# Kernel tuning notes

Measured on AMD Instinct MI355X. Metric: run time of the kernel, lower is better.

The kernel has to match this reference:

```python
import jax, jax.numpy as jnp
import numpy as np

B, N1, N2, D = 4096, 16, 32, 30   # node batch, 1st-hop nbrs, 2nd-hop nbrs, nodeDataLen
H, HD = 6, 5                       # heads, head_dim (embed_dim = size_out*heads = 30)
LH = 64                            # linear_hidden
NEG_SLOPE = 0.02


def setup_inputs() -> dict:
    key = jax.random.key(0)
    ks = jax.random.split(key, 20)
    def w(k, shape, std=0.2):
        return jax.random.normal(k, shape, dtype=jnp.float32) * std
    return {
        "x2": jax.random.normal(ks[0], (B, N1, N2, D), dtype=jnp.float32),
        "self_feat": jax.random.normal(ks[1], (B, D), dtype=jnp.float32),
        # second-hop GraphLayer params (size_in=30 -> embed 30)
        "lin_w2": w(ks[2], (D, D)), "lin_b2": jnp.zeros((D,), jnp.float32),
        "in_w2": w(ks[3], (3 * D, D), 0.1), "in_b2": jnp.zeros((3 * D,), jnp.float32),
        "out_w2": w(ks[4], (D, D), 0.1), "out_b2": jnp.zeros((D,), jnp.float32),
        # first-hop GraphLayer params
        "lin_w1": w(ks[5], (D, D)), "lin_b1": jnp.zeros((D,), jnp.float32),
        "in_w1": w(ks[6], (3 * D, D), 0.1), "in_b1": jnp.zeros((3 * D,), jnp.float32),
        "out_w1": w(ks[7], (D, D), 0.1), "out_b1": jnp.zeros((D,), jnp.float32),
        # classification MLP
        "cw1": w(ks[8], (LH, D), 0.02), "cb1": jnp.zeros((LH,), jnp.float32),
        "cw2": w(ks[9], (LH, LH), 0.02), "cb2": jnp.zeros((LH,), jnp.float32),
        "cw3": w(ks[10], (2, LH), 0.02), "cb3": jnp.zeros((2,), jnp.float32),
    }


def graph_layer(x, lw, lb, iw, ib, ow, ob):
    """x: [S, D] -> Linear + LeakyReLU(0.02) + MHA(self) + mean over S -> [D].
    Dropout(0.2) is identity in eval mode."""
    S = x.shape[0]
    y = jax.nn.leaky_relu(x @ lw.T + lb, NEG_SLOPE)          # [S, D]
    qkv = y @ iw.T + ib                                       # [S, 3D] packed in_proj
    q, k, v = jnp.split(qkv, 3, axis=-1)
    q = q.reshape(S, H, HD)
    k = k.reshape(S, H, HD)
    v = v.reshape(S, H, HD)
    scores = jnp.einsum('shd,thd->hst', q, k) / np.float32(np.sqrt(HD))
    att = jax.nn.softmax(scores, axis=-1)                     # [H, S, S]
    o = jnp.einsum('hst,thd->shd', att, v).reshape(S, H * HD) # [S, D]
    o = o @ ow.T + ob
    return o.mean(axis=0)                                     # [D]


def reference(x2, self_feat,
              lin_w2, lin_b2, in_w2, in_b2, out_w2, out_b2,
              lin_w1, lin_b1, in_w1, in_b1, out_w1, out_b1,
              cw1, cb1, cw2, cb2, cw3, cb3):
    gl2 = lambda x: graph_layer(x, lin_w2, lin_b2, in_w2, in_b2, out_w2, out_b2)
    h1 = jax.vmap(jax.vmap(gl2))(x2)                          # [B, N1, D] second-hop aggregation
    seq = jnp.concatenate([h1, self_feat[:, None, :]], axis=1)  # [B, N1+1, D] append current node
    gl1 = lambda x: graph_layer(x, lin_w1, lin_b1, in_w1, in_b1, out_w1, out_b1)
    emb = jax.vmap(gl1)(seq)                                  # [B, D]
    h = jax.nn.leaky_relu(emb @ cw1.T + cb1, NEG_SLOPE)
    h = jax.nn.leaky_relu(h @ cw2.T + cb2, NEG_SLOPE)
    logits = h @ cw3.T + cb3                                  # [B, 2]
    # original applies Softmax(dim=0) to the 1-D 2-vector per node == softmax over classes
    return jax.nn.softmax(logits, axis=-1)
```

## Files before the change

### kernel.cpp

```cpp
#include <hip/hip_runtime.h>
#include <math.h>

#define LRELU(v) fmaxf((v), 0.02f * (v))

typedef __attribute__((ext_vector_type(8)))  short short8;
typedef __attribute__((ext_vector_type(4)))  float f32x4;
typedef __attribute__((ext_vector_type(16))) float f32x16;
typedef __attribute__((ext_vector_type(2)))  int   int2v;
typedef __attribute__((ext_vector_type(4)))  int   int4v;

__device__ inline short f2bf(float f) {
    unsigned u = __builtin_bit_cast(unsigned, f);
    unsigned r = (u + 0x7FFFu + ((u >> 16) & 1u)) >> 16;
    return (short)r;
}
__device__ inline int cvt_pk_bf16(float lo, float hi) {
    int r;
    asm("v_cvt_pk_bf16_f32 %0, %1, %2" : "=v"(r) : "v"(lo), "v"(hi));
    return r;
}
__device__ inline float exp2_asm(float x) {
    float r;
    asm("v_exp_f32 %0, %1" : "=v"(r) : "v"(x));
    return r;
}

#define PAIRS 8
#define RS5L  0.6451994329f

__global__ __launch_bounds__(256, 5) void gl2_kernel(
    const float* __restrict__ x2,
    const float* __restrict__ lw, const float* __restrict__ lb,
    const float* __restrict__ iw, const float* __restrict__ ib,
    const float* __restrict__ ow, const float* __restrict__ ob,
    float* __restrict__ h1out)
{
    __shared__ __attribute__((aligned(16))) short y_lds[32][40];
    __shared__ __attribute__((aligned(16))) short qmf[6][33][8];
    __shared__ __attribute__((aligned(16))) short kmf[6][33][8];
    __shared__ __attribute__((aligned(16))) short vbf[6][8][40];
    __shared__ float obar[32];

    const int tid  = threadIdx.x;
    const int lane = tid & 63;
    const int w    = tid >> 6;
    const int l15  = lane & 15;
    const int lq   = lane >> 4;
    const int h5   = lane >> 5;
    const int scol = lane & 31;
    const int rowz = (lane < 32) ? scol : 32;

    for (int i = tid; i < 792; i += 256) { ((int*)qmf)[i] = 0; ((int*)kmf)[i] = 0; }
    for (int i = tid; i < 960; i += 256) ((int*)vbf)[i] = 0;
    if (tid < 2) obar[30 + tid] = 0.0f;

    const int di = w & 1, si = w >> 1;
    short8 blw; float lbv;
    {
        int d = di * 16 + l15;
        #pragma unroll
        for (int i = 0; i < 8; ++i) {
            int k = lq * 8 + i;
            blw[i] = f2bf((d < 30 && k < 30) ? lw[d * 30 + k] : 0.0f);
        }
        lbv = (d < 30) ? lb[d] : 0.0f;
    }
    const int jtA = (3 * w) >> 1, jtB = (3 * w + 2) >> 1;
    short8 biwA, biwB; float ibvA, ibvB;
    {
        int jA = jtA * 16 + l15, jB = jtB * 16 + l15;
        #pragma unroll
        for (int i = 0; i < 8; ++i) {
            int k = lq * 8 + i;
            biwA[i] = f2bf((jA < 90 && k < 30) ? iw[jA * 30 + k] : 0.0f);
            biwB[i] = f2bf((jB < 90 && k < 30) ? iw[jB * 30 + k] : 0.0f);
        }
        ibvA = (jA < 90) ? ib[jA] : 0.0f;
        ibvB = (jB < 90) ? ib[jB] : 0.0f;
    }
    __syncthreads();

    for (int p = 0; p < PAIRS; ++p) {
        const long pair = (long)blockIdx.x * PAIRS + p;
        const float* xp = x2 + pair * 960;

        {
            int s = si * 16 + l15;
            const float* xr = xp + s * 30 + lq * 8;
            float xv[8];
            #pragma unroll
            for (int i = 0; i < 8; ++i) {
                int k = lq * 8 + i;
                xv[i] = (k < 30) ? xr[i] : 0.0f;
            }
            int4v ai;
            ai.x = cvt_pk_bf16(xv[0], xv[1]);
            ai.y = cvt_pk_bf16(xv[2], xv[3]);
            ai.z = cvt_pk_bf16(xv[4], xv[5]);
            ai.w = cvt_pk_bf16(xv[6], xv[7]);
            short8 af = __builtin_bit_cast(short8, ai);
            f32x4 c = {0.0f, 0.0f, 0.0f, 0.0f};
            c = __builtin_amdgcn_mfma_f32_16x16x32_bf16(af, blw, c, 0, 0, 0);
            float y0 = LRELU(c[0] + lbv), y1 = LRELU(c[1] + lbv);
            float y2 = LRELU(c[2] + lbv), y3 = LRELU(c[3] + lbv);
            int p01 = cvt_pk_bf16(y0, y1), p23 = cvt_pk_bf16(y2, y3);
            int row = si * 16 + lq * 4, col = di * 16 + l15;
            y_lds[row + 0][col] = (short)p01;
            y_lds[row + 1][col] = (short)(p01 >> 16);
            y_lds[row + 2][col] = (short)p23;
            y_lds[row + 3][col] = (short)(p23 >> 16);
        }
        __syncthreads();

        {
            short8 a0 = *(const short8*)&y_lds[l15][lq * 8];
            short8 a1 = *(const short8*)&y_lds[16 + l15][lq * 8];
            #pragma unroll
            for (int t = 0; t < 3; ++t) {
                int T = 3 * w + t, jt = T >> 1, si_ = T & 1;
                short8 a = si_ ? a1 : a0;
                short8 b = (jt == jtA) ? biwA : biwB;
                float ibv = (jt == jtA) ? ibvA : ibvB;
                f32x4 c = {0.0f, 0.0f, 0.0f, 0.0f};
                c = __builtin_amdgcn_mfma_f32_16x16x32_bf16(a, b, c, 0, 0, 0);
                int j = jt * 16 + l15;
                int s0 = si_ * 16 + lq * 4;
                if (j < 30) {
                    int h = j / 5, e = j - 5 * h;
                    int p01 = cvt_pk_bf16(c[0] + ibv, c[1] + ibv);
                    int p23 = cvt_pk_bf16(c[2] + ibv, c[3] + ibv);
                    qmf[h][s0 + 0][e] = (short)p01;
                    qmf[h][s0 + 1][e] = (short)(p01 >> 16);
                    qmf[h][s0 + 2][e] = (short)p23;
                    qmf[h][s0 + 3][e] = (short)(p23 >> 16);
                } else if (j < 60) {
                    int jj = j - 30; int h = jj / 5, e = jj - 5 * h;
                    float ibl = ibv * RS5L;
                    int p01 = cvt_pk_bf16(fmaf(c[0], RS5L, ibl), fmaf(c[1], RS5L, ibl));
                    int p23 = cvt_pk_bf16(fmaf(c[2], RS5L, ibl), fmaf(c[3], RS5L, ibl));
                    kmf[h][s0 + 0][e] = (short)p01;
                    kmf[h][s0 + 1][e] = (short)(p01 >> 16);
                    kmf[h][s0 + 2][e] = (short)p23;
                    kmf[h][s0 + 3][e] = (short)(p23 >> 16);
                } else if (j < 90) {
                    int jj = j - 60; int h = jj / 5, e = jj - 5 * h;
                    int k0 = ((s0 >> 1) & 4) | ((s0 << 1) & 8) | (s0 & 16);
                    int2v wv;
                    wv.x = cvt_pk_bf16(c[0] + ibv, c[1] + ibv);
                    wv.y = cvt_pk_bf16(c[2] + ibv, c[3] + ibv);
                    *(int2v*)&vbf[h][e][k0] = wv;
                }
            }
        }
        __syncthreads();

        if (w < 3) {
            #pragma unroll
            for (int hh = 0; hh < 2; ++hh) {
                const int h = 2 * w + hh;
                short8 af = *(const short8*)&kmf[h][rowz][0];
                short8 bf = *(const short8*)&qmf[h][rowz][0];
                f32x16 c;
                #pragma unroll
                for (int r = 0; r < 16; ++r) c[r] = 0.0f;
                c = __builtin_amdgcn_mfma_f32_32x32x16_bf16(af, bf, c, 0, 0, 0);
                float m = c[0];
                #pragma unroll
                for (int r = 1; r < 16; ++r) m = fmaxf(m, c[r]);
                m = fmaxf(m, __shfl_xor(m, 32));
                float Z = 0.0f;
                #pragma unroll
                for (int r = 0; r < 16; ++r) { c[r] = exp2_asm(c[r] - m); Z += c[r]; }
                Z += __shfl_xor(Z, 32);
                float rZ = __builtin_amdgcn_rcpf(Z) * (1.0f / 32.0f);
                int4v a1i, a2i;
                a1i.x = cvt_pk_bf16(c[0] * rZ,  c[1] * rZ);
                a1i.y = cvt_pk_bf16(c[2] * rZ,  c[3] * rZ);
                a1i.z = cvt_pk_bf16(c[4] * rZ,  c[5] * rZ);
                a1i.w = cvt_pk_bf16(c[6] * rZ,  c[7] * rZ);
                a2i.x = cvt_pk_bf16(c[8] * rZ,  c[9] * rZ);
                a2i.y = cvt_pk_bf16(c[10] * rZ, c[11] * rZ);
                a2i.z = cvt_pk_bf16(c[12] * rZ, c[13] * rZ);
                a2i.w = cvt_pk_bf16(c[14] * rZ, c[15] * rZ);
                short8 b1 = *(const short8*)&vbf[h][scol & 7][8 * h5];
                short8 b2 = *(const short8*)&vbf[h][scol & 7][16 + 8 * h5];
                f32x16 P;
                #pragma unroll
                for (int r = 0; r < 16; ++r) P[r] = 0.0f;
                P = __builtin_amdgcn_mfma_f32_32x32x16_bf16(
                        __builtin_bit_cast(short8, a1i), b1, P, 0, 0, 0);
                P = __builtin_amdgcn_mfma_f32_32x32x16_bf16(
                        __builtin_bit_cast(short8, a2i), b2, P, 0, 0, 0);
                float sm = 0.0f;
                #pragma unroll
                for (int r = 0; r < 16; ++r) sm += P[r];
                sm += __shfl_xor(sm, 32);
                if (lane < 5) obar[h * 5 + lane] = sm;
            }
        }
        __syncthreads();

        if (tid < 240) {
            const int d = tid >> 3, jq = tid & 7;
            f32x4 ov = *(const f32x4*)&obar[jq * 4];
            float part = 0.0f;
            #pragma unroll
            for (int i = 0; i < 4; ++i) {
                int j = jq * 4 + i;
                if (j < 30) part = fmaf(ov[i], ow[d * 30 + j], part);
            }
            part += __shfl_down(part, 4, 8);
            part += __shfl_down(part, 2, 8);
            part += __shfl_down(part, 1, 8);
            if (jq == 0) h1out[pair * 30 + d] = part + ob[d];
        }
    }
}

__global__ __launch_bounds__(256, 5) void gl1_mlp_kernel(
    const float* __restrict__ h1, const float* __restrict__ self_feat,
    const float* __restrict__ lw, const float* __restrict__ lb,
    const float* __restrict__ iw, const float* __restrict__ ib,
    const float* __restrict__ ow, const float* __restrict__ ob,
    const float* __restrict__ cw1, const float* __restrict__ cb1,
    const float* __restrict__ cw2, const float* __restrict__ cb2,
    const float* __restrict__ cw3, const float* __restrict__ cb3,
    float* __restrict__ out)
{
    __shared__ __attribute__((aligned(16))) short y_lds[32][40];
    __shared__ __attribute__((aligned(16))) short qmf[6][33][8];
    __shared__ __attribute__((aligned(16))) short kmf[6][33][8];
    __shared__ __attribute__((aligned(16))) short vbf[6][8][40];
    __shared__ float obar[32];
    __shared__ float embb[32];
    __shared__ float hb1[64];
    __shared__ float hb2[64];
    __shared__ float lg[2];

    const int tid  = threadIdx.x;
    const int lane = tid & 63;
    const int w    = tid >> 6;
    const int l15  = lane & 15;
    const int lq   = lane >> 4;
    const int h5   = lane >> 5;
    const int scol = lane & 31;
    const int rowz = (lane < 32) ? scol : 32;

    for (int i = tid; i < 792; i += 256) { ((int*)qmf)[i] = 0; ((int*)kmf)[i] = 0; }
    for (int i = tid; i < 960; i += 256) ((int*)vbf)[i] = 0;
    if (tid < 2) obar[30 + tid] = 0.0f;

    const int di = w & 1, si = w >> 1;
    short8 blw; float lbv;
    {
        int d = di * 16 + l15;
        #pragma unroll
        for (int i = 0; i < 8; ++i) {
            int k = lq * 8 + i;
            blw[i] = f2bf((d < 30 && k < 30) ? lw[d * 30 + k] : 0.0f);
        }
        lbv = (d < 30) ? lb[d] : 0.0f;
    }
    const int jtA = (3 * w) >> 1, jtB = (3 * w + 2) >> 1;
    short8 biwA, biwB; float ibvA, ibvB;
    {
        int jA = jtA * 16 + l15, jB = jtB * 16 + l15;
        #pragma unroll
        for (int i = 0; i < 8; ++i) {
            int k = lq * 8 + i;
            biwA[i] = f2bf((jA < 90 && k < 30) ? iw[jA * 30 + k] : 0.0f);
            biwB[i] = f2bf((jB < 90 && k < 30) ? iw[jB * 30 + k] : 0.0f);
        }
        ibvA = (jA < 90) ? ib[jA] : 0.0f;
        ibvB = (jB < 90) ? ib[jB] : 0.0f;
    }
    __syncthreads();

    const long node = (long)blockIdx.x;
    const float* h1p = h1 + node * 480;
    const float* sfp = self_feat + node * 30;

    {
        float xv[8];
        if (si == 0) {
            const float* xr = h1p + l15 * 30 + lq * 8;
            #pragma unroll
            for (int i = 0; i < 8; ++i) {
                int k = lq * 8 + i;
                xv[i] = (k < 30) ? xr[i] : 0.0f;
            }
        } else {
            #pragma unroll
            for (int i = 0; i < 8; ++i) {
                int k = lq * 8 + i;
                xv[i] = (l15 == 0 && k < 30) ? sfp[k] : 0.0f;
            }
        }
        int4v ai;
        ai.x = cvt_pk_bf16(xv[0], xv[1]);
        ai.y = cvt_pk_bf16(xv[2], xv[3]);
        ai.z = cvt_pk_bf16(xv[4], xv[5]);
        ai.w = cvt_pk_bf16(xv[6], xv[7]);
        short8 af = __builtin_bit_cast(short8, ai);
        f32x4 c = {0.0f, 0.0f, 0.0f, 0.0f};
        c = __builtin_amdgcn_mfma_f32_16x16x32_bf16(af, blw, c, 0, 0, 0);
        float y0 = LRELU(c[0] + lbv), y1 = LRELU(c[1] + lbv);
        float y2 = LRELU(c[2] + lbv), y3 = LRELU(c[3] + lbv);
        int p01 = cvt_pk_bf16(y0, y1), p23 = cvt_pk_bf16(y2, y3);
        int row = si * 16 + lq * 4, col = di * 16 + l15;
        y_lds[row + 0][col] = (short)p01;
        y_lds[row + 1][col] = (short)(p01 >> 16);
        y_lds[row + 2][col] = (short)p23;
        y_lds[row + 3][col] = (short)(p23 >> 16);
    }
    __syncthreads();

    {
        short8 a0 = *(const short8*)&y_lds[l15][lq * 8];
        short8 a1 = *(const short8*)&y_lds[16 + l15][lq * 8];
        #pragma unroll
        for (int t = 0; t < 3; ++t) {
            int T = 3 * w + t, jt = T >> 1, si_ = T & 1;
            short8 a = si_ ? a1 : a0;
            short8 b = (jt == jtA) ? biwA : biwB;
            float ibv = (jt == jtA) ? ibvA : ibvB;
            f32x4 c = {0.0f, 0.0f, 0.0f, 0.0f};
            c = __builtin_amdgcn_mfma_f32_16x16x32_bf16(a, b, c, 0, 0, 0);
            int j = jt * 16 + l15;
            int s0 = si_ * 16 + lq * 4;
            if (j < 30) {
                int h = j / 5, e = j - 5 * h;
                int p01 = cvt_pk_bf16(c[0] + ibv, c[1] + ibv);
                int p23 = cvt_pk_bf16(c[2] + ibv, c[3] + ibv);
                qmf[h][s0 + 0][e] = (short)p01;
                qmf[h][s0 + 1][e] = (short)(p01 >> 16);
                qmf[h][s0 + 2][e] = (short)p23;
                qmf[h][s0 + 3][e] = (short)(p23 >> 16);
            } else if (j < 60) {
                int jj = j - 30; int h = jj / 5, e = jj - 5 * h;
                float ibl = ibv * RS5L;
                int p01 = cvt_pk_bf16(fmaf(c[0], RS5L, ibl), fmaf(c[1], RS5L, ibl));
                int p23 = cvt_pk_bf16(fmaf(c[2], RS5L, ibl), fmaf(c[3], RS5L, ibl));
                kmf[h][s0 + 0][e] = (short)p01;
                kmf[h][s0 + 1][e] = (short)(p01 >> 16);
                kmf[h][s0 + 2][e] = (short)p23;
                kmf[h][s0 + 3][e] = (short)(p23 >> 16);
            } else if (j < 90) {
                int jj = j - 60; int h = jj / 5, e = jj - 5 * h;
                int k0 = ((s0 >> 1) & 4) | ((s0 << 1) & 8) | (s0 & 16);
                int2v wv;
                wv.x = cvt_pk_bf16(c[0] + ibv, c[1] + ibv);
                wv.y = cvt_pk_bf16(c[2] + ibv, c[3] + ibv);
                *(int2v*)&vbf[h][e][k0] = wv;
            }
        }
    }
    __syncthreads();

    if (w < 3) {
        #pragma unroll
        for (int hh = 0; hh < 2; ++hh) {
            const int h = 2 * w + hh;
            short8 af = *(const short8*)&kmf[h][rowz][0];
            short8 bf = *(const short8*)&qmf[h][rowz][0];
            f32x16 c;
            #pragma unroll
            for (int r = 0; r < 16; ++r) c[r] = 0.0f;
            c = __builtin_amdgcn_mfma_f32_32x32x16_bf16(af, bf, c, 0, 0, 0);
            #pragma unroll
            for (int r = 0; r < 16; ++r) {
                int tr = (r & 3) + 8 * (r >> 2) + 4 * h5;
                c[r] = (tr < 17) ? c[r] : -1e30f;
            }
            float m = c[0];
            #pragma unroll
            for (int r = 1; r < 16; ++r) m = fmaxf(m, c[r]);
            m = fmaxf(m, __shfl_xor(m, 32));
            float Z = 0.0f;
            #pragma unroll
            for (int r = 0; r < 16; ++r) { c[r] = exp2_asm(c[r] - m); Z += c[r]; }
            Z += __shfl_xor(Z, 32);
            float rZ = __builtin_amdgcn_rcpf(Z) * (1.0f / 17.0f);
            int4v a1i, a2i;
            a1i.x = cvt_pk_bf16(c[0] * rZ,  c[1] * rZ);
            a1i.y = cvt_pk_bf16(c[2] * rZ,  c[3] * rZ);
            a1i.z = cvt_pk_bf16(c[4] * rZ,  c[5] * rZ);
            a1i.w = cvt_pk_bf16(c[6] * rZ,  c[7] * rZ);
            a2i.x = cvt_pk_bf16(c[8] * rZ,  c[9] * rZ);
            a2i.y = cvt_pk_bf16(c[10] * rZ, c[11] * rZ);
            a2i.z = cvt_pk_bf16(c[12] * rZ, c[13] * rZ);
            a2i.w = cvt_pk_bf16(c[14] * rZ, c[15] * rZ);
            short8 b1 = *(const short8*)&vbf[h][scol & 7][8 * h5];
            short8 b2 = *(const short8*)&vbf[h][scol & 7][16 + 8 * h5];
            f32x16 P;
            #pragma unroll
            for (int r = 0; r < 16; ++r) P[r] = 0.0f;
            P = __builtin_amdgcn_mfma_f32_32x32x16_bf16(
                    __builtin_bit_cast(short8, a1i), b1, P, 0, 0, 0);
            P = __builtin_amdgcn_mfma_f32_32x32x16_bf16(
                    __builtin_bit_cast(short8, a2i), b2, P, 0, 0, 0);
            float sm = 0.0f;
            #pragma unroll
            for (int r = 0; r < 8; ++r) sm += P[r];
            sm += (h5 == 0) ? P[8] : 0.0f;
            sm += __shfl_xor(sm, 32);
            if (lane < 5) obar[h * 5 + lane] = sm;
        }
    }
    __syncthreads();

    if (tid < 240) {
        const int d = tid >> 3, jq = tid & 7;
        f32x4 ov = *(const f32x4*)&obar[jq * 4];
        float part = 0.0f;
        #pragma unroll
        for (int i = 0; i < 4; ++i) {
            int j = jq * 4 + i;
            if (j < 30) part = fmaf(ov[i], ow[d * 30 + j], part);
        }
        part += __shfl_down(part, 4, 8);
        part += __shfl_down(part, 2, 8);
        part += __shfl_down(part, 1, 8);
        if (jq == 0) embb[d] = part + ob[d];
    }
    __syncthreads();

    {
        const int o = tid >> 2, kq = tid & 3;
        float part = 0.0f;
        #pragma unroll
        for (int i = 0; i < 8; ++i) {
            int k = kq * 8 + i;
            if (k < 30) part = fmaf(embb[k], cw1[o * 30 + k], part);
        }
        part += __shfl_down(part, 2, 4);
        part += __shfl_down(part, 1, 4);
        if (kq == 0) hb1[o] = LRELU(part + cb1[o]);
    }
    __syncthreads();
    {
        const int o = tid >> 2, kq = tid & 3;
        float part = 0.0f;
        #pragma unroll
        for (int i = 0; i < 16; ++i) {
            int k = kq * 16 + i;
            part = fmaf(hb1[k], cw2[o * 64 + k], part);
        }
        part += __shfl_down(part, 2, 4);
        part += __shfl_down(part, 1, 4);
        if (kq == 0) hb2[o] = LRELU(part + cb2[o]);
    }
    __syncthreads();
    if (tid < 128) {
        const int c = tid >> 6, k = tid & 63;
        float part = hb2[k] * cw3[c * 64 + k];
        part += __shfl_down(part, 32);
        part += __shfl_down(part, 16);
        part += __shfl_down(part, 8);
        part += __shfl_down(part, 4);
        part += __shfl_down(part, 2);
        part += __shfl_down(part, 1);
        if (k == 0) lg[c] = part + cb3[c];
    }
    __syncthreads();
    if (tid < 2) {
        float m = fmaxf(lg[0], lg[1]);
        float e0 = __expf(lg[0] - m), e1 = __expf(lg[1] - m);
        float pr = ((tid == 0) ? e0 : e1) / (e0 + e1);
        out[node * 2 + tid] = pr;
    }
}

extern "C" void kernel_launch(void* const* d_in, const int* in_sizes, int n_in,
                              void* d_out, int out_size, void* d_ws, size_t ws_size,
                              hipStream_t stream)
{
    const float* x2        = (const float*)d_in[0];
    const float* self_feat = (const float*)d_in[1];
    const float* lin_w2 = (const float*)d_in[2];
    const float* lin_b2 = (const float*)d_in[3];
    const float* in_w2  = (const float*)d_in[4];
    const float* in_b2  = (const float*)d_in[5];
    const float* out_w2 = (const float*)d_in[6];
    const float* out_b2 = (const float*)d_in[7];
    const float* lin_w1 = (const float*)d_in[8];
    const float* lin_b1 = (const float*)d_in[9];
    const float* in_w1  = (const float*)d_in[10];
    const float* in_b1  = (const float*)d_in[11];
    const float* out_w1 = (const float*)d_in[12];
    const float* out_b1 = (const float*)d_in[13];
    const float* cw1 = (const float*)d_in[14];
    const float* cb1 = (const float*)d_in[15];
    const float* cw2 = (const float*)d_in[16];
    const float* cb2 = (const float*)d_in[17];
    const float* cw3 = (const float*)d_in[18];
    const float* cb3 = (const float*)d_in[19];
    float* outp = (float*)d_out;

    float* h1 = (float*)d_ws;

    gl2_kernel<<<(4096 * 16) / PAIRS, 256, 0, stream>>>(
        x2, lin_w2, lin_b2, in_w2, in_b2, out_w2, out_b2, h1);

    gl1_mlp_kernel<<<4096, 256, 0, stream>>>(
        h1, self_feat, lin_w1, lin_b1, in_w1, in_b1, out_w1, out_b1,
        cw1, cb1, cw2, cb2, cw3, cb3, outp);
}
```

Baseline: 547.1 us.

## Fuse second-hop, first-hop and MLP kernels into one per-node kernel

Merges the two launches into one kernel where each block handles a whole node: it processes its 16 neighbour sets two at a time, with double-width LDS buffers so all four waves share the attention stage (three heads each instead of two heads on three waves). The h1 results stay in shared memory rather than going through a global workspace, and the first-hop layer and MLP then run in the same block. This removes one kernel launch and the h1 write/read round trip, and raises wave utilisation in the attention stage. In exchange it doubles LDS use and adds register pressure from holding both layers' weights, which may lower occupancy.

Result: slower. 585.3 us (+7.0%).

```diff
diff --git a/kernel.cpp b/kernel.cpp
--- a/kernel.cpp
+++ b/kernel.cpp
@@ -25,21 +25,31 @@
     return r;
 }
 
-#define PAIRS 8
 #define RS5L  0.6451994329f
 
-__global__ __launch_bounds__(256, 5) void gl2_kernel(
-    const float* __restrict__ x2,
-    const float* __restrict__ lw, const float* __restrict__ lb,
-    const float* __restrict__ iw, const float* __restrict__ ib,
-    const float* __restrict__ ow, const float* __restrict__ ob,
-    float* __restrict__ h1out)
+__global__ __launch_bounds__(256, 5) void fused_kernel(
+    const float* __restrict__ x2, const float* __restrict__ self_feat,
+    const float* __restrict__ lw2, const float* __restrict__ lb2,
+    const float* __restrict__ iw2, const float* __restrict__ ib2,
+    const float* __restrict__ ow2, const float* __restrict__ ob2,
+    const float* __restrict__ lw1, const float* __restrict__ lb1,
+    const float* __restrict__ iw1, const float* __restrict__ ib1,
+    const float* __restrict__ ow1, const float* __restrict__ ob1,
+    const float* __restrict__ cw1, const float* __restrict__ cb1,
+    const float* __restrict__ cw2, const float* __restrict__ cb2,
+    const float* __restrict__ cw3, const float* __restrict__ cb3,
+    float* __restrict__ out)
 {
-    __shared__ __attribute__((aligned(16))) short y_lds[32][40];
-    __shared__ __attribute__((aligned(16))) short qmf[6][33][8];
-    __shared__ __attribute__((aligned(16))) short kmf[6][33][8];
-    __shared__ __attribute__((aligned(16))) short vbf[6][8][40];
-    __shared__ float obar[32];
+    __shared__ __attribute__((aligned(16))) short y_lds[2][32][40];
+    __shared__ __attribute__((aligned(16))) short qmf[2][6][33][8];
+    __shared__ __attribute__((aligned(16))) short kmf[2][6][33][8];
+    __shared__ __attribute__((aligned(16))) short vbf[2][6][8][40];
+    __shared__ __attribute__((aligned(16))) float h1f[16][33];
+    __shared__ float obar[2][32];
+    __shared__ float embb[32];
+    __shared__ float hb1[64];
+    __shared__ float hb2[64];
+    __shared__ float lg[2];
 
     const int tid  = threadIdx.x;
     const int lane = tid & 63;
@@ -50,116 +60,134 @@
     const int scol = lane & 31;
     const int rowz = (lane < 32) ? scol : 32;
 
-    for (int i = tid; i < 792; i += 256) { ((int*)qmf)[i] = 0; ((int*)kmf)[i] = 0; }
-    for (int i = tid; i < 960; i += 256) ((int*)vbf)[i] = 0;
-    if (tid < 2) obar[30 + tid] = 0.0f;
+    for (int i = tid; i < 1584; i += 256) { ((int*)qmf)[i] = 0; ((int*)kmf)[i] = 0; }
+    for (int i = tid; i < 1920; i += 256) ((int*)vbf)[i] = 0;
+    if (tid < 4) obar[tid >> 1][30 + (tid & 1)] = 0.0f;
 
     const int di = w & 1, si = w >> 1;
-    short8 blw; float lbv;
+    short8 blw2f, blw1f; float lbv2v, lbv1v;
     {
         int d = di * 16 + l15;
         #pragma unroll
         for (int i = 0; i < 8; ++i) {
             int k = lq * 8 + i;
-            blw[i] = f2bf((d < 30 && k < 30) ? lw[d * 30 + k] : 0.0f);
-        }
-        lbv = (d < 30) ? lb[d] : 0.0f;
+            bool ok = (d < 30 && k < 30);
+            blw2f[i] = f2bf(ok ? lw2[d * 30 + k] : 0.0f);
+            blw1f[i] = f2bf(ok ? lw1[d * 30 + k] : 0.0f);
+        }
+        lbv2v = (d < 30) ? lb2[d] : 0.0f;
+        lbv1v = (d < 30) ? lb1[d] : 0.0f;
     }
     const int jtA = (3 * w) >> 1, jtB = (3 * w + 2) >> 1;
-    short8 biwA, biwB; float ibvA, ibvB;
+    short8 biwA2, biwB2, biwA1, biwB1;
+    float ibvA2, ibvB2, ibvA1, ibvB1;
     {
         int jA = jtA * 16 + l15, jB = jtB * 16 + l15;
         #pragma unroll
         for (int i = 0; i < 8; ++i) {
             int k = lq * 8 + i;
-            biwA[i] = f2bf((jA < 90 && k < 30) ? iw[jA * 30 + k] : 0.0f);
-            biwB[i] = f2bf((jB < 90 && k < 30) ? iw[jB * 30 + k] : 0.0f);
-        }
-        ibvA = (jA < 90) ? ib[jA] : 0.0f;
-        ibvB = (jB < 90) ? ib[jB] : 0.0f;
-    }
-    __syncthreads();
-
-    for (int p = 0; p < PAIRS; ++p) {
-        const long pair = (long)blockIdx.x * PAIRS + p;
-        const float* xp = x2 + pair * 960;
+            bool okA = (jA < 90 && k < 30), okB = (jB < 90 && k < 30);
+            biwA2[i] = f2bf(okA ? iw2[jA * 30 + k] : 0.0f);
+            biwB2[i] = f2bf(okB ? iw2[jB * 30 + k] : 0.0f);
+            biwA1[i] = f2bf(okA ? iw1[jA * 30 + k] : 0.0f);
+            biwB1[i] = f2bf(okB ? iw1[jB * 30 + k] : 0.0f);
+        }
+        ibvA2 = (jA < 90) ? ib2[jA] : 0.0f;
+        ibvB2 = (jB < 90) ? ib2[jB] : 0.0f;
+        ibvA1 = (jA < 90) ? ib1[jA] : 0.0f;
+        ibvB1 = (jB < 90) ? ib1[jB] : 0.0f;
+    }
+    __syncthreads();
+
+    const long node = (long)blockIdx.x;
+    const float* xbase = x2 + node * (16L * 960);
+    const float* sfp   = self_feat + node * 30;
+
+    for (int it = 0; it < 8; ++it) {
 
         {
             int s = si * 16 + l15;
-            const float* xr = xp + s * 30 + lq * 8;
-            float xv[8];
-            #pragma unroll
-            for (int i = 0; i < 8; ++i) {
-                int k = lq * 8 + i;
-                xv[i] = (k < 30) ? xr[i] : 0.0f;
-            }
-            int4v ai;
-            ai.x = cvt_pk_bf16(xv[0], xv[1]);
-            ai.y = cvt_pk_bf16(xv[2], xv[3]);
-            ai.z = cvt_pk_bf16(xv[4], xv[5]);
-            ai.w = cvt_pk_bf16(xv[6], xv[7]);
-            short8 af = __builtin_bit_cast(short8, ai);
-            f32x4 c = {0.0f, 0.0f, 0.0f, 0.0f};
-            c = __builtin_amdgcn_mfma_f32_16x16x32_bf16(af, blw, c, 0, 0, 0);
-            float y0 = LRELU(c[0] + lbv), y1 = LRELU(c[1] + lbv);
-            float y2 = LRELU(c[2] + lbv), y3 = LRELU(c[3] + lbv);
-            int p01 = cvt_pk_bf16(y0, y1), p23 = cvt_pk_bf16(y2, y3);
-            int row = si * 16 + lq * 4, col = di * 16 + l15;
-            y_lds[row + 0][col] = (short)p01;
-            y_lds[row + 1][col] = (short)(p01 >> 16);
-            y_lds[row + 2][col] = (short)p23;
-            y_lds[row + 3][col] = (short)(p23 >> 16);
+            #pragma unroll
+            for (int pr = 0; pr < 2; ++pr) {
+                const float* xr = xbase + (2 * it + pr) * 960 + s * 30 + lq * 8;
+                float xv[8];
+                #pragma unroll
+                for (int i = 0; i < 8; ++i) {
+                    int k = lq * 8 + i;
+                    xv[i] = (k < 30) ? xr[i] : 0.0f;
+                }
+                int4v ai;
+                ai.x = cvt_pk_bf16(xv[0], xv[1]);
+                ai.y = cvt_pk_bf16(xv[2], xv[3]);
+                ai.z = cvt_pk_bf16(xv[4], xv[5]);
+                ai.w = cvt_pk_bf16(xv[6], xv[7]);
+                short8 af = __builtin_bit_cast(short8, ai);
+                f32x4 c = {0.0f, 0.0f, 0.0f, 0.0f};
+                c = __builtin_amdgcn_mfma_f32_16x16x32_bf16(af, blw2f, c, 0, 0, 0);
+                float y0 = LRELU(c[0] + lbv2v), y1 = LRELU(c[1] + lbv2v);
+                float y2 = LRELU(c[2] + lbv2v), y3 = LRELU(c[3] + lbv2v);
+                int p01 = cvt_pk_bf16(y0, y1), p23 = cvt_pk_bf16(y2, y3);
+                int row = si * 16 + lq * 4, col = di * 16 + l15;
+                y_lds[pr][row + 0][col] = (short)p01;
+                y_lds[pr][row + 1][col] = (short)(p01 >> 16);
+                y_lds[pr][row + 2][col] = (short)p23;
+                y_lds[pr][row + 3][col] = (short)(p23 >> 16);
+            }
         }
         __syncthreads();
 
         {
-            short8 a0 = *(const short8*)&y_lds[l15][lq * 8];
-            short8 a1 = *(const short8*)&y_lds[16 + l15][lq * 8];
-            #pragma unroll
-            for (int t = 0; t < 3; ++t) {
-                int T = 3 * w + t, jt = T >> 1, si_ = T & 1;
-                short8 a = si_ ? a1 : a0;
-                short8 b = (jt == jtA) ? biwA : biwB;
-                float ibv = (jt == jtA) ? ibvA : ibvB;
-                f32x4 c = {0.0f, 0.0f, 0.0f, 0.0f};
-                c = __builtin_amdgcn_mfma_f32_16x16x32_bf16(a, b, c, 0, 0, 0);
-                int j = jt * 16 + l15;
-                int s0 = si_ * 16 + lq * 4;
-                if (j < 30) {
-                    int h = j / 5, e = j - 5 * h;
-                    int p01 = cvt_pk_bf16(c[0] + ibv, c[1] + ibv);
-                    int p23 = cvt_pk_bf16(c[2] + ibv, c[3] + ibv);
-                    qmf[h][s0 + 0][e] = (short)p01;
-                    qmf[h][s0 + 1][e] = (short)(p01 >> 16);
-                    qmf[h][s0 + 2][e] = (short)p23;
-                    qmf[h][s0 + 3][e] = (short)(p23 >> 16);
-                } else if (j < 60) {
-                    int jj = j - 30; int h = jj / 5, e = jj - 5 * h;
-                    float ibl = ibv * RS5L;
-                    int p01 = cvt_pk_bf16(fmaf(c[0], RS5L, ibl), fmaf(c[1], RS5L, ibl));
-                    int p23 = cvt_pk_bf16(fmaf(c[2], RS5L, ibl), fmaf(c[3], RS5L, ibl));
-                    kmf[h][s0 + 0][e] = (short)p01;
-                    kmf[h][s0 + 1][e] = (short)(p01 >> 16);
-                    kmf[h][s0 + 2][e] = (short)p23;
-                    kmf[h][s0 + 3][e] = (short)(p23 >> 16);
-                } else if (j < 90) {
-                    int jj = j - 60; int h = jj / 5, e = jj - 5 * h;
-                    int k0 = ((s0 >> 1) & 4) | ((s0 << 1) & 8) | (s0 & 16);
-                    int2v wv;
-                    wv.x = cvt_pk_bf16(c[0] + ibv, c[1] + ibv);
-                    wv.y = cvt_pk_bf16(c[2] + ibv, c[3] + ibv);
-                    *(int2v*)&vbf[h][e][k0] = wv;
+            #pragma unroll
+            for (int pr = 0; pr < 2; ++pr) {
+                short8 a0 = *(const short8*)&y_lds[pr][l15][lq * 8];
+                short8 a1 = *(const short8*)&y_lds[pr][16 + l15][lq * 8];
+                #pragma unroll
+                for (int t = 0; t < 3; ++t) {
+                    int T = 3 * w + t, jt = T >> 1, si_ = T & 1;
+                    short8 a = si_ ? a1 : a0;
+                    short8 b = (jt == jtA) ? biwA2 : biwB2;
+                    float ibv = (jt == jtA) ? ibvA2 : ibvB2;
+                    f32x4 c = {0.0f, 0.0f, 0.0f, 0.0f};
+                    c = __builtin_amdgcn_mfma_f32_16x16x32_bf16(a, b, c, 0, 0, 0);
+                    int j = jt * 16 + l15;
+                    int s0 = si_ * 16 + lq * 4;
+                    if (j < 30) {
+                        int h = j / 5, e = j - 5 * h;
+                        int p01 = cvt_pk_bf16(c[0] + ibv, c[1] + ibv);
+                        int p23 = cvt_pk_bf16(c[2] + ibv, c[3] + ibv);
+                        qmf[pr][h][s0 + 0][e] = (short)p01;
+                        qmf[pr][h][s0 + 1][e] = (short)(p01 >> 16);
+                        qmf[pr][h][s0 + 2][e] = (short)p23;
+                        qmf[pr][h][s0 + 3][e] = (short)(p23 >> 16);
+                    } else if (j < 60) {
+                        int jj = j - 30; int h = jj / 5, e = jj - 5 * h;
+                        float ibl = ibv * RS5L;
+                        int p01 = cvt_pk_bf16(fmaf(c[0], RS5L, ibl), fmaf(c[1], RS5L, ibl));
+                        int p23 = cvt_pk_bf16(fmaf(c[2], RS5L, ibl), fmaf(c[3], RS5L, ibl));
+                        kmf[pr][h][s0 + 0][e] = (short)p01;
+                        kmf[pr][h][s0 + 1][e] = (short)(p01 >> 16);
+                        kmf[pr][h][s0 + 2][e] = (short)p23;
+                        kmf[pr][h][s0 + 3][e] = (short)(p23 >> 16);
+                    } else if (j < 90) {
+                        int jj = j - 60; int h = jj / 5, e = jj - 5 * h;
+                        int k0 = ((s0 >> 1) & 4) | ((s0 << 1) & 8) | (s0 & 16);
+                        int2v wv;
+                        wv.x = cvt_pk_bf16(c[0] + ibv, c[1] + ibv);
+                        wv.y = cvt_pk_bf16(c[2] + ibv, c[3] + ibv);
+                        *(int2v*)&vbf[pr][h][e][k0] = wv;
+                    }
                 }
             }
         }
         __syncthreads();
 
-        if (w < 3) {
-            #pragma unroll
-            for (int hh = 0; hh < 2; ++hh) {
-                const int h = 2 * w + hh;
-                short8 af = *(const short8*)&kmf[h][rowz][0];
-                short8 bf = *(const short8*)&qmf[h][rowz][0];
+        {
+            const int pr = w >> 1;
+            #pragma unroll
+            for (int hh = 0; hh < 3; ++hh) {
+                const int h = 3 * (w & 1) + hh;
+                short8 af = *(const short8*)&kmf[pr][h][rowz][0];
+                short8 bf = *(const short8*)&qmf[pr][h][rowz][0];
                 f32x16 c;
                 #pragma unroll
                 for (int r = 0; r < 16; ++r) c[r] = 0.0f;
@@ -182,8 +210,8 @@
                 a2i.y = cvt_pk_bf16(c[10] * rZ, c[11] * rZ);
                 a2i.z = cvt_pk_bf16(c[12] * rZ, c[13] * rZ);
                 a2i.w = cvt_pk_bf16(c[14] * rZ, c[15] * rZ);
-                short8 b1 = *(const short8*)&vbf[h][scol & 7][8 * h5];
-                short8 b2 = *(const short8*)&vbf[h][scol & 7][16 + 8 * h5];
+                short8 b1 = *(const short8*)&vbf[pr][h][scol & 7][8 * h5];
+                short8 b2 = *(const short8*)&vbf[pr][h][scol & 7][16 + 8 * h5];
                 f32x16 P;
                 #pragma unroll
                 for (int r = 0; r < 16; ++r) P[r] = 0.0f;
@@ -195,99 +223,39 @@
                 #pragma unroll
                 for (int r = 0; r < 16; ++r) sm += P[r];
                 sm += __shfl_xor(sm, 32);
-                if (lane < 5) obar[h * 5 + lane] = sm;
+                if (lane < 5) obar[pr][h * 5 + lane] = sm;
             }
         }
         __syncthreads();
 
         if (tid < 240) {
             const int d = tid >> 3, jq = tid & 7;
-            f32x4 ov = *(const f32x4*)&obar[jq * 4];
-            float part = 0.0f;
-            #pragma unroll
-            for (int i = 0; i < 4; ++i) {
-                int j = jq * 4 + i;
-                if (j < 30) part = fmaf(ov[i], ow[d * 30 + j], part);
-            }
-            part += __shfl_down(part, 4, 8);
-            part += __shfl_down(part, 2, 8);
-            part += __shfl_down(part, 1, 8);
-            if (jq == 0) h1out[pair * 30 + d] = part + ob[d];
-        }
-    }
-}
-
-__global__ __launch_bounds__(256, 5) void gl1_mlp_kernel(
-    const float* __restrict__ h1, const float* __restrict__ self_feat,
-    const float* __restrict__ lw, const float* __restrict__ lb,
-    const float* __restrict__ iw, const float* __restrict__ ib,
-    const float* __restrict__ ow, const float* __restrict__ ob,
-    const float* __restrict__ cw1, const float* __restrict__ cb1,
-    const float* __restrict__ cw2, const float* __restrict__ cb2,
-    const float* __restrict__ cw3, const float* __restrict__ cb3,
-    float* __restrict__ out)
-{
-    __shared__ __attribute__((aligned(16))) short y_lds[32][40];
-    __shared__ __attribute__((aligned(16))) short qmf[6][33][8];
-    __shared__ __attribute__((aligned(16))) short kmf[6][33][8];
-    __shared__ __attribute__((aligned(16))) short vbf[6][8][40];
-    __shared__ float obar[32];
-    __shared__ float embb[32];
-    __shared__ float hb1[64];
-    __shared__ float hb2[64];
-    __shared__ float lg[2];
-
-    const int tid  = threadIdx.x;
-    const int lane = tid & 63;
-    const int w    = tid >> 6;
-    const int l15  = lane & 15;
-    const int lq   = lane >> 4;
-    const int h5   = lane >> 5;
-    const int scol = lane & 31;
-    const int rowz = (lane < 32) ? scol : 32;
-
-    for (int i = tid; i < 792; i += 256) { ((int*)qmf)[i] = 0; ((int*)kmf)[i] = 0; }
-    for (int i = tid; i < 960; i += 256) ((int*)vbf)[i] = 0;
-    if (tid < 2) obar[30 + tid] = 0.0f;
-
-    const int di = w & 1, si = w >> 1;
-    short8 blw; float lbv;
-    {
-        int d = di * 16 + l15;
-        #pragma unroll
-        for (int i = 0; i < 8; ++i) {
-            int k = lq * 8 + i;
-            blw[i] = f2bf((d < 30 && k < 30) ? lw[d * 30 + k] : 0.0f);
-        }
-        lbv = (d < 30) ? lb[d] : 0.0f;
-    }
-    const int jtA = (3 * w) >> 1, jtB = (3 * w + 2) >> 1;
-    short8 biwA, biwB; float ibvA, ibvB;
-    {
-        int jA = jtA * 16 + l15, jB = jtB * 16 + l15;
-        #pragma unroll
-        for (int i = 0; i < 8; ++i) {
-            int k = lq * 8 + i;
-            biwA[i] = f2bf((jA < 90 && k < 30) ? iw[jA * 30 + k] : 0.0f);
-            biwB[i] = f2bf((jB < 90 && k < 30) ? iw[jB * 30 + k] : 0.0f);
-        }
-        ibvA = (jA < 90) ? ib[jA] : 0.0f;
-        ibvB = (jB < 90) ? ib[jB] : 0.0f;
-    }
-    __syncthreads();
-
-    const long node = (long)blockIdx.x;
-    const float* h1p = h1 + node * 480;
-    const float* sfp = self_feat + node * 30;
+            #pragma unroll
+            for (int pr = 0; pr < 2; ++pr) {
+                f32x4 ov = *(const f32x4*)&obar[pr][jq * 4];
+                float part = 0.0f;
+                #pragma unroll
+                for (int i = 0; i < 4; ++i) {
+                    int j = jq * 4 + i;
+                    if (j < 30) part = fmaf(ov[i], ow2[d * 30 + j], part);
+                }
+                part += __shfl_down(part, 4, 8);
+                part += __shfl_down(part, 2, 8);
+                part += __shfl_down(part, 1, 8);
+                if (jq == 0) h1f[2 * it + pr][d] = part + ob2[d];
+            }
+        }
+    }
+    __syncthreads();
+
 
     {
         float xv[8];
         if (si == 0) {
-            const float* xr = h1p + l15 * 30 + lq * 8;
             #pragma unroll
             for (int i = 0; i < 8; ++i) {
                 int k = lq * 8 + i;
-                xv[i] = (k < 30) ? xr[i] : 0.0f;
+                xv[i] = (k < 30) ? h1f[l15][k] : 0.0f;
             }
         } else {
             #pragma unroll
@@ -303,27 +271,27 @@
         ai.w = cvt_pk_bf16(xv[6], xv[7]);
         short8 af = __builtin_bit_cast(short8, ai);
         f32x4 c = {0.0f, 0.0f, 0.0f, 0.0f};
-        c = __builtin_amdgcn_mfma_f32_16x16x32_bf16(af, blw, c, 0, 0, 0);
-        float y0 = LRELU(c[0] + lbv), y1 = LRELU(c[1] + lbv);
-        float y2 = LRELU(c[2] + lbv), y3 = LRELU(c[3] + lbv);
+        c = __builtin_amdgcn_mfma_f32_16x16x32_bf16(af, blw1f, c, 0, 0, 0);
+        float y0 = LRELU(c[0] + lbv1v), y1 = LRELU(c[1] + lbv1v);
+        float y2 = LRELU(c[2] + lbv1v), y3 = LRELU(c[3] + lbv1v);
         int p01 = cvt_pk_bf16(y0, y1), p23 = cvt_pk_bf16(y2, y3);
         int row = si * 16 + lq * 4, col = di * 16 + l15;
-        y_lds[row + 0][col] = (short)p01;
-        y_lds[row + 1][col] = (short)(p01 >> 16);
-        y_lds[row + 2][col] = (short)p23;
-        y_lds[row + 3][col] = (short)(p23 >> 16);
-    }
-    __syncthreads();
-
-    {
-        short8 a0 = *(const short8*)&y_lds[l15][lq * 8];
-        short8 a1 = *(const short8*)&y_lds[16 + l15][lq * 8];
+        y_lds[0][row + 0][col] = (short)p01;
+        y_lds[0][row + 1][col] = (short)(p01 >> 16);
+        y_lds[0][row + 2][col] = (short)p23;
+        y_lds[0][row + 3][col] = (short)(p23 >> 16);
+    }
+    __syncthreads();
+
+    {
+        short8 a0 = *(const short8*)&y_lds[0][l15][lq * 8];
+        short8 a1 = *(const short8*)&y_lds[0][16 + l15][lq * 8];
         #pragma unroll
         for (int t = 0; t < 3; ++t) {
             int T = 3 * w + t, jt = T >> 1, si_ = T & 1;
             short8 a = si_ ? a1 : a0;
-            short8 b = (jt == jtA) ? biwA : biwB;
-            float ibv = (jt == jtA) ? ibvA : ibvB;
+            short8 b = (jt == jtA) ? biwA1 : biwB1;
+            float ibv = (jt == jtA) ? ibvA1 : ibvB1;
             f32x4 c = {0.0f, 0.0f, 0.0f, 0.0f};
             c = __builtin_amdgcn_mfma_f32_16x16x32_bf16(a, b, c, 0, 0, 0);
             int j = jt * 16 + l15;
@@ -332,26 +300,26 @@
                 int h = j / 5, e = j - 5 * h;
                 int p01 = cvt_pk_bf16(c[0] + ibv, c[1] + ibv);
                 int p23 = cvt_pk_bf16(c[2] + ibv, c[3] + ibv);
-                qmf[h][s0 + 0][e] = (short)p01;
-                qmf[h][s0 + 1][e] = (short)(p01 >> 16);
-                qmf[h][s0 + 2][e] = (short)p23;
-                qmf[h][s0 + 3][e] = (short)(p23 >> 16);
+                qmf[0][h][s0 + 0][e] = (short)p01;
+                qmf[0][h][s0 + 1][e] = (short)(p01 >> 16);
+                qmf[0][h][s0 + 2][e] = (short)p23;
+                qmf[0][h][s0 + 3][e] = (short)(p23 >> 16);
             } else if (j < 60) {
                 int jj = j - 30; int h = jj / 5, e = jj - 5 * h;
                 float ibl = ibv * RS5L;
                 int p01 = cvt_pk_bf16(fmaf(c[0], RS5L, ibl), fmaf(c[1], RS5L, ibl));
                 int p23 = cvt_pk_bf16(fmaf(c[2], RS5L, ibl), fmaf(c[3], RS5L, ibl));
-                kmf[h][s0 + 0][e] = (short)p01;
-                kmf[h][s0 + 1][e] = (short)(p01 >> 16);
-                kmf[h][s0 + 2][e] = (short)p23;
-                kmf[h][s0 + 3][e] = (short)(p23 >> 16);
+                kmf[0][h][s0 + 0][e] = (short)p01;
+                kmf[0][h][s0 + 1][e] = (short)(p01 >> 16);
+                kmf[0][h][s0 + 2][e] = (short)p23;
+                kmf[0][h][s0 + 3][e] = (short)(p23 >> 16);
             } else if (j < 90) {
                 int jj = j - 60; int h = jj / 5, e = jj - 5 * h;
                 int k0 = ((s0 >> 1) & 4) | ((s0 << 1) & 8) | (s0 & 16);
                 int2v wv;
                 wv.x = cvt_pk_bf16(c[0] + ibv, c[1] + ibv);
                 wv.y = cvt_pk_bf16(c[2] + ibv, c[3] + ibv);
-                *(int2v*)&vbf[h][e][k0] = wv;
+                *(int2v*)&vbf[0][h][e][k0] = wv;
             }
         }
     }
@@ -361,8 +329,8 @@
         #pragma unroll
         for (int hh = 0; hh < 2; ++hh) {
             const int h = 2 * w + hh;
-            short8 af = *(const short8*)&kmf[h][rowz][0];
-            short8 bf = *(const short8*)&qmf[h][rowz][0];
+            short8 af = *(const short8*)&kmf[0][h][rowz][0];
+            short8 bf = *(const short8*)&qmf[0][h][rowz][0];
             f32x16 c;
             #pragma unroll
             for (int r = 0; r < 16; ++r) c[r] = 0.0f;
@@ -390,8 +358,8 @@
             a2i.y = cvt_pk_bf16(c[10] * rZ, c[11] * rZ);
             a2i.z = cvt_pk_bf16(c[12] * rZ, c[13] * rZ);
             a2i.w = cvt_pk_bf16(c[14] * rZ, c[15] * rZ);
-            short8 b1 = *(const short8*)&vbf[h][scol & 7][8 * h5];
-            short8 b2 = *(const short8*)&vbf[h][scol & 7][16 + 8 * h5];
+            short8 b1 = *(const short8*)&vbf[0][h][scol & 7][8 * h5];
+            short8 b2 = *(const short8*)&vbf[0][h][scol & 7][16 + 8 * h5];
             f32x16 P;
             #pragma unroll
             for (int r = 0; r < 16; ++r) P[r] = 0.0f;
@@ -404,24 +372,24 @@
             for (int r = 0; r < 8; ++r) sm += P[r];
             sm += (h5 == 0) ? P[8] : 0.0f;
             sm += __shfl_xor(sm, 32);
-            if (lane < 5) obar[h * 5 + lane] = sm;
+            if (lane < 5) obar[0][h * 5 + lane] = sm;
         }
     }
     __syncthreads();
 
     if (tid < 240) {
         const int d = tid >> 3, jq = tid & 7;
-        f32x4 ov = *(const f32x4*)&obar[jq * 4];
+        f32x4 ov = *(const f32x4*)&obar[0][jq * 4];
         float part = 0.0f;
         #pragma unroll
         for (int i = 0; i < 4; ++i) {
             int j = jq * 4 + i;
-            if (j < 30) part = fmaf(ov[i], ow[d * 30 + j], part);
+            if (j < 30) part = fmaf(ov[i], ow1[d * 30 + j], part);
         }
         part += __shfl_down(part, 4, 8);
         part += __shfl_down(part, 2, 8);
         part += __shfl_down(part, 1, 8);
-        if (jq == 0) embb[d] = part + ob[d];
+        if (jq == 0) embb[d] = part + ob1[d];
     }
     __syncthreads();
 
@@ -497,12 +465,9 @@
     const float* cb3 = (const float*)d_in[19];
     float* outp = (float*)d_out;
 
-    float* h1 = (float*)d_ws;
-
-    gl2_kernel<<<(4096 * 16) / PAIRS, 256, 0, stream>>>(
-        x2, lin_w2, lin_b2, in_w2, in_b2, out_w2, out_b2, h1);
-
-    gl1_mlp_kernel<<<4096, 256, 0, stream>>>(
-        h1, self_feat, lin_w1, lin_b1, in_w1, in_b1, out_w1, out_b1,
+    fused_kernel<<<4096, 256, 0, stream>>>(
+        x2, self_feat,
+        lin_w2, lin_b2, in_w2, in_b2, out_w2, out_b2,
+        lin_w1, lin_b1, in_w1, in_b1, out_w1, out_b1,
         cw1, cb1, cw2, cb2, cw3, cb3, outp);
 }
```
